# Optimization experiments

Hardware: AMD Instinct MI355X
Metric: run time of the kernel (lower is better)

Reference implementation:

```python
import jax, jax.numpy as jnp
import numpy as np


def setup_inputs() -> dict:
    key = jax.random.key(0)
    k1, k2, k3, k4 = jax.random.split(key, 4)
    B, A, E, K, H = 256, 64, 128, 6, 256
    return {
        "bond_representations": jax.random.normal(k1, (1, B, E, H), dtype=jnp.float32),
        "bond_pairs": jax.random.randint(k2, (B, E, 2), 0, A, dtype=jnp.int32),
        "bond_neighbors": jax.random.randint(k3, (B, E, K), 0, E, dtype=jnp.int32),
        "xyz": jax.random.normal(k4, (B, A, 3), dtype=jnp.float32),
    }


def _distance_weight(xyz, bond_pairs):
    # xyz: [B, A, 3]; bond_pairs: [B, E, 2] -> gathered [B, E, 2, 3]
    d = jax.vmap(lambda x, p: x[p])(xyz, bond_pairs)
    diff = d[:, :, 0, :] - d[:, :, 1, :]          # [B, E, 3]
    d2 = jnp.sum(diff * diff, axis=-1)            # [B, E]
    inv = 1.0 / d2                                # squared-distance reciprocal weight
    return jnp.where(jnp.isinf(inv), jnp.zeros_like(inv), inv)


def reference(bond_representations, bond_pairs, bond_neighbors, xyz):
    # include_3d=True, mean_readout=False (sum readout)
    dist = _distance_weight(xyz, bond_pairs)                       # [B, E]
    weighted = dist[None, :, :, None] * bond_representations      # [1, B, E, H]
    wb = weighted[0]                                               # [B, E, H]
    # gather neighbor bond features: [B, E, K, H], then sum over K
    nbf = jax.vmap(lambda w, nb: w[nb])(wb, bond_neighbors)
    msg = jnp.sum(nbf, axis=2)                                     # [B, E, H]
    return msg[None]                                               # [1, B, E, H]
```

## Files before the change

### kernel.cpp

```cpp
#include <hip/hip_runtime.h>
#include <math.h>

#define NB 256
#define NA 64
#define NE 128
#define NK 6
#define NH 256

__global__ __launch_bounds__(256) void edge_msg_kernel(
    const float* __restrict__ rep,
    const int*   __restrict__ pairs,
    const int*   __restrict__ nbrs,
    const float* __restrict__ xyz,
    float*       __restrict__ out)
{
    const int b   = blockIdx.y;
    const int e0  = blockIdx.x * 4;
    const int tid = threadIdx.x;

    __shared__ float sw[4][NK];
    __shared__ int   snb[4][NK];

    if (tid < 4 * NK) {
        const int se = tid / NK;
        const int k  = tid % NK;
        const int e  = e0 + se;
        const int nb = nbrs[(b * NE + e) * NK + k];
        const int p0 = pairs[(b * NE + nb) * 2 + 0];
        const int p1 = pairs[(b * NE + nb) * 2 + 1];
        const float* x0 = xyz + ((size_t)b * NA + p0) * 3;
        const float* x1 = xyz + ((size_t)b * NA + p1) * 3;
        const float dx = x0[0] - x1[0];
        const float dy = x0[1] - x1[1];
        const float dz = x0[2] - x1[2];
        const float d2 = dx * dx + dy * dy + dz * dz;
        float inv = 1.0f / d2;
        if (isinf(inv)) inv = 0.0f;
        sw[se][k]  = inv;
        snb[se][k] = nb;
    }
    __syncthreads();

    const int se   = tid >> 6;
    const int lane = tid & 63;

    const float4* rep4 = (const float4*)(rep + (size_t)b * NE * NH);
    float4 acc = make_float4(0.f, 0.f, 0.f, 0.f);
#pragma unroll
    for (int k = 0; k < NK; ++k) {
        const float  w = sw[se][k];
        const float4 v = rep4[snb[se][k] * (NH / 4) + lane];
        acc.x += w * v.x;
        acc.y += w * v.y;
        acc.z += w * v.z;
        acc.w += w * v.w;
    }
    float4* out4 = (float4*)(out + ((size_t)b * NE + (e0 + se)) * NH);
    out4[lane] = acc;
}

extern "C" void kernel_launch(void* const* d_in, const int* in_sizes, int n_in,
                              void* d_out, int out_size, void* d_ws, size_t ws_size,
                              hipStream_t stream) {
    const float* rep   = (const float*)d_in[0];
    const int*   pairs = (const int*)  d_in[1];
    const int*   nbrs  = (const int*)  d_in[2];
    const float* xyz   = (const float*)d_in[3];
    float*       out   = (float*)d_out;

    dim3 grid(NE / 4, NB);
    dim3 block(256);
    edge_msg_kernel<<<grid, block, 0, stream>>>(rep, pairs, nbrs, xyz, out);
}
```

Before: 102.1 us.

## Stage whole per-batch bond representation tile in LDS, one block per batch

After: 95.07 us. 6.9% less time.

```diff
diff --git a/kernel.cpp b/kernel.cpp
--- a/kernel.cpp
+++ b/kernel.cpp
@@ -7,27 +7,28 @@
 #define NK 6
 #define NH 256
 
-__global__ __launch_bounds__(256) void edge_msg_kernel(
+__global__ __launch_bounds__(256, 1) void edge_msg_kernel(
     const float* __restrict__ rep,
     const int*   __restrict__ pairs,
     const int*   __restrict__ nbrs,
     const float* __restrict__ xyz,
     float*       __restrict__ out)
 {
-    const int b   = blockIdx.y;
-    const int e0  = blockIdx.x * 4;
+    extern __shared__ float smem[];
+    float* s_rep = smem;
+    float* s_w   = smem + NE * NH;
+    int*   s_nb  = (int*)(s_w + NE);
+
+    const int b   = blockIdx.x;
     const int tid = threadIdx.x;
 
-    __shared__ float sw[4][NK];
-    __shared__ int   snb[4][NK];
+    const int* nbr_b = nbrs + b * NE * NK;
+#pragma unroll
+    for (int i = tid; i < NE * NK; i += 256) s_nb[i] = nbr_b[i];
 
-    if (tid < 4 * NK) {
-        const int se = tid / NK;
-        const int k  = tid % NK;
-        const int e  = e0 + se;
-        const int nb = nbrs[(b * NE + e) * NK + k];
-        const int p0 = pairs[(b * NE + nb) * 2 + 0];
-        const int p1 = pairs[(b * NE + nb) * 2 + 1];
+    if (tid < NE) {
+        const int p0 = pairs[(b * NE + tid) * 2 + 0];
+        const int p1 = pairs[(b * NE + tid) * 2 + 1];
         const float* x0 = xyz + ((size_t)b * NA + p0) * 3;
         const float* x1 = xyz + ((size_t)b * NA + p1) * 3;
         const float dx = x0[0] - x1[0];
@@ -36,27 +37,42 @@
         const float d2 = dx * dx + dy * dy + dz * dz;
         float inv = 1.0f / d2;
         if (isinf(inv)) inv = 0.0f;
-        sw[se][k]  = inv;
-        snb[se][k] = nb;
+        s_w[tid] = inv;
+    }
+
+    const float4* g4 = (const float4*)(rep + (size_t)b * NE * NH);
+    float4*       l4 = (float4*)s_rep;
+#pragma unroll
+    for (int i = 0; i < 32; i += 8) {
+        float4 r[8];
+#pragma unroll
+        for (int j = 0; j < 8; ++j) r[j] = g4[tid + (i + j) * 256];
+#pragma unroll
+        for (int j = 0; j < 8; ++j) l4[tid + (i + j) * 256] = r[j];
     }
     __syncthreads();
 
-    const int se   = tid >> 6;
+    const int wid  = tid >> 6;
     const int lane = tid & 63;
+    const float4* lrep4 = (const float4*)s_rep;
+    float4* outb = (float4*)(out + (size_t)b * NE * NH);
 
-    const float4* rep4 = (const float4*)(rep + (size_t)b * NE * NH);
-    float4 acc = make_float4(0.f, 0.f, 0.f, 0.f);
+#pragma unroll 4
+    for (int ei = 0; ei < 32; ++ei) {
+        const int e = wid * 32 + ei;
+        float4 acc = make_float4(0.f, 0.f, 0.f, 0.f);
 #pragma unroll
-    for (int k = 0; k < NK; ++k) {
-        const float  w = sw[se][k];
-        const float4 v = rep4[snb[se][k] * (NH / 4) + lane];
-        acc.x += w * v.x;
-        acc.y += w * v.y;
-        acc.z += w * v.z;
-        acc.w += w * v.w;
+        for (int k = 0; k < NK; ++k) {
+            const int   nb = s_nb[e * NK + k];
+            const float w  = s_w[nb];
+            const float4 v = lrep4[nb * (NH / 4) + lane];
+            acc.x += w * v.x;
+            acc.y += w * v.y;
+            acc.z += w * v.z;
+            acc.w += w * v.w;
+        }
+        outb[e * (NH / 4) + lane] = acc;
     }
-    float4* out4 = (float4*)(out + ((size_t)b * NE + (e0 + se)) * NH);
-    out4[lane] = acc;
 }
 
 extern "C" void kernel_launch(void* const* d_in, const int* in_sizes, int n_in,
@@ -68,7 +84,7 @@
     const float* xyz   = (const float*)d_in[3];
     float*       out   = (float*)d_out;
 
-    dim3 grid(NE / 4, NB);
-    dim3 block(256);
-    edge_msg_kernel<<<grid, block, 0, stream>>>(rep, pairs, nbrs, xyz, out);
+    const size_t lds_bytes = (size_t)(NE * NH + NE) * sizeof(float)
+                           + (size_t)(NE * NK) * sizeof(int);
+    edge_msg_kernel<<<dim3(NB), dim3(256), lds_bytes, stream>>>(rep, pairs, nbrs, xyz, out);
 }
```
